# Optimization experiments

Hardware: AMD Instinct MI355X
Metric: run time of the kernel (lower is better)

Reference implementation:

```python
import jax, jax.numpy as jnp
import numpy as np

N = 100000
E = 6400000
IN_CH = 128
HID = 8
HEADS = 2
OUT_CH = 1
NEG_SLOPE = 0.2


def gat_conv(x, src, dst, W, a_src, a_dst, bias, heads, out_ch, concat, n_nodes):
    # x: [N, F_in], W: [F_in, heads*out_ch], a_src/a_dst: [heads, out_ch]
    h = (x @ W).reshape(n_nodes, heads, out_ch)          # [N, H, C]
    alpha_s = jnp.sum(h * a_src[None], axis=-1)          # [N, H]
    alpha_d = jnp.sum(h * a_dst[None], axis=-1)          # [N, H]
    alpha = alpha_s[src] + alpha_d[dst]                  # [E, H]
    alpha = jax.nn.leaky_relu(alpha, NEG_SLOPE)
    # segment softmax over incoming edges of each destination node
    seg_max = jax.ops.segment_max(alpha, dst, num_segments=n_nodes)  # [N, H]
    alpha = jnp.exp(alpha - seg_max[dst])
    denom = jax.ops.segment_sum(alpha, dst, num_segments=n_nodes)    # [N, H]
    alpha = alpha / (denom[dst] + 1e-16)
    msg = h[src] * alpha[..., None]                       # [E, H, C]
    out = jax.ops.segment_sum(msg, dst, num_segments=n_nodes)        # [N, H, C]
    if concat:
        out = out.reshape(n_nodes, heads * out_ch)
    else:
        out = out.mean(axis=1)
    return out + bias


def setup_inputs() -> dict:
    key = jax.random.key(0)
    ks = jax.random.split(key, 12)
    x = jax.random.normal(ks[0], (N, IN_CH), dtype=jnp.float32)
    edge_index = jax.random.randint(ks[1], (2, E), 0, N, dtype=jnp.int64)
    s1 = 1.0 / np.sqrt(IN_CH)
    W1 = jax.random.normal(ks[2], (IN_CH, HEADS * HID), dtype=jnp.float32) * s1
    a_src1 = jax.random.normal(ks[3], (HEADS, HID), dtype=jnp.float32) * (1.0 / np.sqrt(HID))
    a_dst1 = jax.random.normal(ks[4], (HEADS, HID), dtype=jnp.float32) * (1.0 / np.sqrt(HID))
    b1 = jnp.zeros((HEADS * HID,), dtype=jnp.float32)
    s2 = 1.0 / np.sqrt(HEADS * HID)
    W2 = jax.random.normal(ks[5], (HEADS * HID, OUT_CH), dtype=jnp.float32) * s2
    a_src2 = jax.random.normal(ks[6], (1, OUT_CH), dtype=jnp.float32)
    a_dst2 = jax.random.normal(ks[7], (1, OUT_CH), dtype=jnp.float32)
    b2 = jnp.zeros((OUT_CH,), dtype=jnp.float32)
    return {"x": x, "edge_index": edge_index, "W1": W1, "a_src1": a_src1,
            "a_dst1": a_dst1, "b1": b1, "W2": W2, "a_src2": a_src2,
            "a_dst2": a_dst2, "b2": b2}


def reference(x, edge_index, W1, a_src1, a_dst1, b1, W2, a_src2, a_dst2, b2):
    # add self-loops (PyG GATConv default)
    loops = jnp.arange(N, dtype=edge_index.dtype)
    src = jnp.concatenate([edge_index[0], loops])
    dst = jnp.concatenate([edge_index[1], loops])
    h = gat_conv(x, src, dst, W1, a_src1, a_dst1, b1, HEADS, HID, True, N)
    h = jax.nn.relu(h)
    out = gat_conv(h, src, dst, W2, a_src2, a_dst2, b2, 1, OUT_CH, False, N)
    return out
```

## Files before the change

### kernel.cpp

```cpp
#include <hip/hip_runtime.h>
#include <hip/hip_fp16.h>
#include <cstdint>
#include <cstddef>

#define N_NODES 100000
#define E_EDGES 6400000
#define E_TOT   (E_EDGES + N_NODES)
#define IN_CH   128
#define NHID    16
#define RECB    64
#define BSHIFT  8
#define BSZ     256
#define NBUCK   391
#define CHUNK   6144
#define BCAP    24
#define NCHUNK  ((E_TOT + CHUNK - 1) / CHUNK)
#define LCAP    18176

__global__ void k_detect(const int* __restrict__ edge, int* __restrict__ flag) {
    if (blockIdx.x == 0 && threadIdx.x == 0) {
        int odd_or = 0;
        for (int i = 0; i < 64; i++) odd_or |= edge[2 * i + 1];
        flag[0] = (odd_or == 0) ? 1 : 0;
    }
}

__global__ __launch_bounds__(256) void k_gemm1(
        const float* __restrict__ x, const float* __restrict__ W1,
        const float* __restrict__ a_src1, const float* __restrict__ a_dst1,
        char* __restrict__ rec, float* __restrict__ adst) {
    __shared__ __align__(16) float sW[IN_CH * NHID];
    __shared__ __align__(16) float sx[16][132];
    __shared__ float sh[16][17];
    int t = threadIdx.x;
    int r = t >> 4, c = t & 15;
    int row = blockIdx.x * 16 + r;

    const float4* W4 = (const float4*)W1;
    ((float4*)sW)[t] = W4[t];
    ((float4*)sW)[t + 256] = W4[t + 256];

    if (row < N_NODES) {
        const float4* xr = (const float4*)(x + (size_t)row * IN_CH);
        float4 v0 = xr[c];
        float4 v1 = xr[c + 16];
        *(float4*)&sx[r][4 * c] = v0;
        *(float4*)&sx[r][64 + 4 * c] = v1;
    }
    __syncthreads();

    float acc = 0.f;
    if (row < N_NODES) {
        #pragma unroll 16
        for (int k = 0; k < IN_CH; k++) acc = fmaf(sx[r][k], sW[k * NHID + c], acc);
        ((__half*)(rec + (size_t)row * RECB))[c] = __float2half(acc);
    }
    sh[r][c] = acc;
    __syncthreads();

    if (row < N_NODES && c < 4) {
        int h = c & 1;
        const float* av = (c >= 2) ? a_dst1 : a_src1;
        float s = 0.f;
        #pragma unroll
        for (int q = 0; q < 8; q++) s = fmaf(sh[r][h * 8 + q], av[h * 8 + q], s);
        if (c < 2) ((float*)(rec + (size_t)row * RECB + 32))[c] = s;
        else       adst[2 * (size_t)row + (c - 2)] = s;
    }
}

__global__ __launch_bounds__(256) void k_ccount(const int* __restrict__ edge,
                                                const int* __restrict__ flag,
                                                int* __restrict__ ccnt) {
    __shared__ int sc[NBUCK];
    int m64 = flag[0];
    int t = threadIdx.x;
    for (int i = t; i < NBUCK; i += 256) sc[i] = 0;
    __syncthreads();
    size_t c0 = (size_t)blockIdx.x * CHUNK;
    size_t cend = c0 + CHUNK; if (cend > E_TOT) cend = E_TOT;
    size_t ee = (cend < (size_t)E_EDGES) ? cend : (size_t)E_EDGES;

    if (m64) {
        const int4* dp = (const int4*)(edge + 2 * (size_t)E_EDGES);
        for (size_t i = c0 + 2 * t; i < ee; i += 512) {
            int4 v = dp[i >> 1];
            atomicAdd(&sc[v.x >> BSHIFT], 1);
            if (i + 1 < ee) atomicAdd(&sc[v.z >> BSHIFT], 1);
        }
    } else {
        const int4* dp = (const int4*)(edge + (size_t)E_EDGES);
        for (size_t i = c0 + 4 * t; i < ee; i += 1024) {
            int4 v = dp[i >> 2];
            atomicAdd(&sc[v.x >> BSHIFT], 1);
            if (i + 1 < ee) atomicAdd(&sc[v.y >> BSHIFT], 1);
            if (i + 2 < ee) atomicAdd(&sc[v.z >> BSHIFT], 1);
            if (i + 3 < ee) atomicAdd(&sc[v.w >> BSHIFT], 1);
        }
    }
    size_t sl0 = (c0 > (size_t)E_EDGES) ? c0 : (size_t)E_EDGES;
    for (size_t i = sl0 + t; i < cend; i += 256) {
        int d = (int)(i - E_EDGES);
        atomicAdd(&sc[d >> BSHIFT], 1);
    }
    __syncthreads();
    for (int i = t; i < NBUCK; i += 256)
        ccnt[(size_t)blockIdx.x * NBUCK + i] = sc[i];
}

__global__ __launch_bounds__(256) void k_cscan(int* __restrict__ ccnt,
                                               int* __restrict__ bcnt) {
    __shared__ int sd[256];
    __shared__ int carry;
    int b = blockIdx.x, t = threadIdx.x;
    if (t == 0) carry = 0;
    __syncthreads();
    for (int base = 0; base < NCHUNK; base += 256) {
        int c = base + t;
        int v = (c < NCHUNK) ? ccnt[(size_t)c * NBUCK + b] : 0;
        sd[t] = v;
        __syncthreads();
        for (int ofs = 1; ofs < 256; ofs <<= 1) {
            int a = sd[t];
            int bb = (t >= ofs) ? sd[t - ofs] : 0;
            __syncthreads();
            sd[t] = a + bb;
            __syncthreads();
        }
        if (c < NCHUNK) ccnt[(size_t)c * NBUCK + b] = sd[t] - v + carry;
        __syncthreads();
        if (t == 255) carry += sd[255];
        __syncthreads();
    }
    if (t == 0) bcnt[b] = carry;
}

__global__ __launch_bounds__(512) void k_bscan(const int* __restrict__ bcnt,
                                               int* __restrict__ bbase) {
    __shared__ int sd[512];
    int t = threadIdx.x;
    int v = (t < NBUCK) ? bcnt[t] : 0;
    sd[t] = v;
    __syncthreads();
    for (int ofs = 1; ofs < 512; ofs <<= 1) {
        int a = sd[t];
        int b = (t >= ofs) ? sd[t - ofs] : 0;
        __syncthreads();
        sd[t] = a + b;
        __syncthreads();
    }
    if (t < NBUCK) bbase[t] = sd[t] - v;
    if (t == NBUCK) bbase[NBUCK] = sd[NBUCK - 1];
}

__global__ __launch_bounds__(256) void k_bin(const int* __restrict__ edge,
                                             const int* __restrict__ flag,
                                             const int* __restrict__ ccnt,
                                             const int* __restrict__ bbase,
                                             unsigned* __restrict__ staged) {
    __shared__ unsigned lbin[NBUCK][BCAP];
    __shared__ int lcnt[NBUCK];
    __shared__ int lbase[NBUCK];
    int m64 = flag[0];
    int t = threadIdx.x;
    int g = t >> 4, lane = t & 15;

    size_t c0 = (size_t)blockIdx.x * CHUNK;
    if (c0 >= E_TOT) return;
    size_t cend = c0 + CHUNK; if (cend > E_TOT) cend = E_TOT;
    size_t ee = (cend < (size_t)E_EDGES) ? cend : (size_t)E_EDGES;

    for (int i = t; i < NBUCK; i += 256) {
        lcnt[i] = 0;
        lbase[i] = bbase[i] + ccnt[(size_t)blockIdx.x * NBUCK + i];
    }
    __syncthreads();

    auto put = [&](int s, int d) {
        int b = d >> BSHIFT;
        unsigned v = (unsigned)s | ((unsigned)(d & (BSZ - 1)) << 17);
        int idx = atomicAdd(&lcnt[b], 1);
        if (idx < BCAP) lbin[b][idx] = v;
        else            staged[lbase[b] + idx] = v;
    };

    if (m64) {
        const int4* sp = (const int4*)edge;
        const int4* dp = (const int4*)(edge + 2 * (size_t)E_EDGES);
        for (size_t i = c0 + 2 * t; i < ee; i += 512) {
            int4 sv = sp[i >> 1];
            int4 dv = dp[i >> 1];
            put(sv.x, dv.x);
            if (i + 1 < ee) put(sv.z, dv.z);
        }
    } else {
        const int4* sp = (const int4*)edge;
        const int4* dp = (const int4*)(edge + (size_t)E_EDGES);
        for (size_t i = c0 + 4 * t; i < ee; i += 1024) {
            int4 sv = sp[i >> 2];
            int4 dv = dp[i >> 2];
            put(sv.x, dv.x);
            if (i + 1 < ee) put(sv.y, dv.y);
            if (i + 2 < ee) put(sv.z, dv.z);
            if (i + 3 < ee) put(sv.w, dv.w);
        }
    }
    size_t sl0 = (c0 > (size_t)E_EDGES) ? c0 : (size_t)E_EDGES;
    for (size_t i = sl0 + t; i < cend; i += 256) {
        int d = (int)(i - E_EDGES);
        put(d, d);
    }
    __syncthreads();
    for (int b = g; b < NBUCK; b += 16) {
        int n = min(lcnt[b], BCAP);
        if (!n) continue;
        int pos = lbase[b];
        for (int i = lane; i < n; i += 16) staged[pos + i] = lbin[b][i];
    }
}

__global__ __launch_bounds__(512) void k_fused1(
        const unsigned* __restrict__ staged, const int* __restrict__ bbase,
        const char* __restrict__ rec, const float* __restrict__ adst,
        const float* __restrict__ b1, const float* __restrict__ W2,
        int* __restrict__ csr, int* __restrict__ offs,
        float* __restrict__ h2out) {
    __shared__ int lcsr[LCAP];
    __shared__ int hist[BSZ];
    __shared__ int segbeg[BSZ];
    __shared__ int cur[BSZ];
    __shared__ float2 sadp[BSZ];
    int bkt = blockIdx.x;
    int t = threadIdx.x;
    int dbase = bkt << BSHIFT;
    int beg = bbase[bkt], end = bbase[bkt + 1];

    if (t < BSZ) {
        hist[t] = 0;
        int d = dbase + t;
        sadp[t] = (d < N_NODES) ? ((const float2*)adst)[d] : make_float2(0.f, 0.f);
    }
    __syncthreads();
    for (int e = beg + t; e < end; e += 512)
        atomicAdd(&hist[staged[e] >> 17], 1);
    __syncthreads();

    int myv = (t < BSZ) ? hist[t] : 0;
    __syncthreads();
    for (int ofs = 1; ofs < BSZ; ofs <<= 1) {
        int a = 0, b = 0;
        if (t < BSZ) { a = hist[t]; b = (t >= ofs) ? hist[t - ofs] : 0; }
        __syncthreads();
        if (t < BSZ) hist[t] = a + b;
        __syncthreads();
    }
    if (t < BSZ) {
        int excl = hist[t] - myv;
        segbeg[t] = excl;
        cur[t] = excl;
        int d = dbase + t;
        if (d < N_NODES) offs[d] = beg + excl;
    }
    if (bkt == NBUCK - 1 && t == 0) offs[N_NODES] = E_TOT;
    __syncthreads();

    for (int e = beg + t; e < end; e += 512) {
        unsigned v = staged[e];
        int pos = atomicAdd(&cur[v >> 17], 1);
        lcsr[pos] = (int)(v & 0x1FFFFu);
    }
    __syncthreads();

    int n = end - beg;
    for (int i = t; i < n; i += 512) csr[beg + i] = lcsr[i];

    int p = t >> 1, sub = t & 1;
    int sb = segbeg[p], se = cur[p];
    float adpv = sub ? sadp[p].y : sadp[p].x;

    float acc[8];
    #pragma unroll
    for (int c = 0; c < 8; c++) acc[c] = 0.f;
    float den = 0.f;

    auto loadslot = [&](int i, float& aspv, float4& hv) {
        if (i < se) {
            int s = lcsr[i];
            const char* rp = rec + (size_t)s * RECB;
            hv = *(const float4*)(rp + sub * 16);
            aspv = *(const float*)(rp + 32 + 4 * sub);
        }
    };
    auto consume = [&](float aspv, const float4& hv) {
        float a = aspv + adpv; a = (a > 0.f) ? a : 0.2f * a;
        float pw = __expf(a);
        den += pw;
        const __half2* hh = (const __half2*)&hv;
        #pragma unroll
        for (int q = 0; q < 4; q++) {
            float2 f = __half22float2(hh[q]);
            acc[2 * q]     = fmaf(pw, f.x, acc[2 * q]);
            acc[2 * q + 1] = fmaf(pw, f.y, acc[2 * q + 1]);
        }
    };

    float aA = 0.f, aB = 0.f, aC = 0.f, aD = 0.f;
    float4 z4 = make_float4(0.f, 0.f, 0.f, 0.f);
    float4 hA = z4, hB = z4, hC = z4, hD = z4;

    int i = sb;
    loadslot(i,     aA, hA);
    loadslot(i + 1, aB, hB);
    loadslot(i + 2, aC, hC);
    loadslot(i + 3, aD, hD);
    while (true) {
        if (i >= se) break;
        consume(aA, hA); loadslot(i + 4, aA, hA); i++;
        if (i >= se) break;
        consume(aB, hB); loadslot(i + 4, aB, hB); i++;
        if (i >= se) break;
        consume(aC, hC); loadslot(i + 4, aC, hC); i++;
        if (i >= se) break;
        consume(aD, hD); loadslot(i + 4, aD, hD); i++;
    }

    float inv = 1.f / (den + 1e-16f);
    float v = 0.f;
    #pragma unroll
    for (int ch = 0; ch < 8; ch++) {
        float o = acc[ch] * inv + b1[8 * sub + ch];
        o = (o > 0.f) ? o : 0.f;
        v = fmaf(o, W2[8 * sub + ch], v);
    }
    v += __shfl_xor(v, 1, 64);
    if (sub == 0) {
        int d = dbase + p;
        if (d < N_NODES) h2out[d] = v;
    }
}

__global__ __launch_bounds__(256) void k_edge2(
        const int* __restrict__ offs, const int* __restrict__ csr,
        const float* __restrict__ h2,
        const float* __restrict__ a_src2, const float* __restrict__ a_dst2,
        const float* __restrict__ b2, float* __restrict__ out) {
    int t = threadIdx.x;
    int g = t >> 4, lane = t & 15;
    int d = blockIdx.x * 16 + g;
    if (d >= N_NODES) return;

    float as2 = a_src2[0], ad2 = a_dst2[0];
    float adv = h2[d] * ad2;
    int beg = offs[d], end = offs[d + 1];

    float den = 0.f, acc = 0.f;
    auto ls = [&](int ee, float& hs) { if (ee < end) hs = h2[csr[ee]]; };
    auto cs = [&](float hs) {
        float a = fmaf(hs, as2, adv);
        a = (a > 0.f) ? a : 0.2f * a;
        float p = __expf(a);
        den += p;
        acc = fmaf(p, hs, acc);
    };
    float hA = 0.f, hB = 0.f, hC = 0.f, hD = 0.f, hE = 0.f, hF = 0.f;
    int e = beg + lane;
    ls(e, hA); ls(e + 16, hB); ls(e + 32, hC);
    ls(e + 48, hD); ls(e + 64, hE); ls(e + 80, hF);
    while (true) {
        if (e >= end) break;
        cs(hA); ls(e + 96, hA); e += 16;
        if (e >= end) break;
        cs(hB); ls(e + 96, hB); e += 16;
        if (e >= end) break;
        cs(hC); ls(e + 96, hC); e += 16;
        if (e >= end) break;
        cs(hD); ls(e + 96, hD); e += 16;
        if (e >= end) break;
        cs(hE); ls(e + 96, hE); e += 16;
        if (e >= end) break;
        cs(hF); ls(e + 96, hF); e += 16;
    }
    #pragma unroll
    for (int m = 1; m < 16; m <<= 1) {
        den += __shfl_xor(den, m, 64);
        acc += __shfl_xor(acc, m, 64);
    }
    if (lane == 0) out[d] = acc / (den + 1e-16f) + b2[0];
}

extern "C" void kernel_launch(void* const* d_in, const int* in_sizes, int n_in,
                              void* d_out, int out_size, void* d_ws, size_t ws_size,
                              hipStream_t stream) {
    const float* x      = (const float*)d_in[0];
    const int*   edge   = (const int*)  d_in[1];
    const float* W1     = (const float*)d_in[2];
    const float* a_src1 = (const float*)d_in[3];
    const float* a_dst1 = (const float*)d_in[4];
    const float* b1     = (const float*)d_in[5];
    const float* W2     = (const float*)d_in[6];
    const float* a_src2 = (const float*)d_in[7];
    const float* a_dst2 = (const float*)d_in[8];
    const float* b2     = (const float*)d_in[9];

    constexpr size_t A = 256;
    auto al = [](size_t b) { return (b + A - 1) / A * A; };
    char* ws = (char*)d_ws;
    size_t off = 0;
    int*      flag   = (int*)(ws + off);      off += al(256);
    int*      ccnt   = (int*)(ws + off);      off += al((size_t)NCHUNK * NBUCK * 4);
    int*      bcnt   = (int*)(ws + off);      off += al(NBUCK * 4);
    int*      bbase  = (int*)(ws + off);      off += al((NBUCK + 1) * 4);
    unsigned* staged = (unsigned*)(ws + off); off += al((size_t)E_TOT * 4);
    int*      csr    = (int*)(ws + off);      off += al((size_t)E_TOT * 4);
    int*      offs   = (int*)(ws + off);      off += al((size_t)(N_NODES + 1) * 4);
    char*     rec    = (char*)(ws + off);     off += al((size_t)N_NODES * RECB);
    float*    adst   = (float*)(ws + off);    off += al((size_t)N_NODES * 2 * 4);
    float*    h2     = (float*)(ws + off);    off += al((size_t)N_NODES * 4);
    (void)ws_size; (void)in_sizes; (void)n_in; (void)out_size;

    k_detect<<<1, 64, 0, stream>>>(edge, flag);
    k_gemm1 <<<(N_NODES + 15) / 16, 256, 0, stream>>>(x, W1, a_src1, a_dst1, rec, adst);
    k_ccount<<<NCHUNK, 256, 0, stream>>>(edge, flag, ccnt);
    k_cscan <<<NBUCK, 256, 0, stream>>>(ccnt, bcnt);
    k_bscan <<<1, 512, 0, stream>>>(bcnt, bbase);
    k_bin   <<<NCHUNK, 256, 0, stream>>>(edge, flag, ccnt, bbase, staged);
    k_fused1<<<NBUCK, 512, 0, stream>>>(staged, bbase, rec, adst, b1, W2, csr, offs, h2);
    k_edge2 <<<(N_NODES + 15) / 16, 256, 0, stream>>>(offs, csr, h2, a_src2, a_dst2, b2,
                                                      (float*)d_out);
}
```

Baseline: 201.8 us.

## Split node records into compact arrays and use smaller buckets with four lanes per node

Replaces the 64-byte padded per-node record with a dense 32-byte fp16 feature array plus a separate float2 source-score array, which cuts the bytes touched per gathered edge. Halves the destination bucket size to 128 nodes, giving twice as many blocks in the fused aggregation kernel, and uses four threads per node with four channels each. Chunk, bin capacity and scan sizes are retuned to match, and a second shuffle reduces across the four lanes. Each source gather now takes two separate loads instead of one record load, and the binning kernel keeps more, smaller buckets in shared memory.

After: 222.1 us. 1.1x slower.

```diff
diff --git a/kernel.cpp b/kernel.cpp
--- a/kernel.cpp
+++ b/kernel.cpp
@@ -8,14 +8,13 @@
 #define E_TOT   (E_EDGES + N_NODES)
 #define IN_CH   128
 #define NHID    16
-#define RECB    64
-#define BSHIFT  8
-#define BSZ     256
-#define NBUCK   391
-#define CHUNK   6144
-#define BCAP    24
+#define BSHIFT  7
+#define BSZ     128
+#define NBUCK   782
+#define CHUNK   4096
+#define BCAP    12
 #define NCHUNK  ((E_TOT + CHUNK - 1) / CHUNK)
-#define LCAP    18176
+#define LCAP    9280
 
 __global__ void k_detect(const int* __restrict__ edge, int* __restrict__ flag) {
     if (blockIdx.x == 0 && threadIdx.x == 0) {
@@ -28,7 +27,8 @@
 __global__ __launch_bounds__(256) void k_gemm1(
         const float* __restrict__ x, const float* __restrict__ W1,
         const float* __restrict__ a_src1, const float* __restrict__ a_dst1,
-        char* __restrict__ rec, float* __restrict__ adst) {
+        __half* __restrict__ h16, float* __restrict__ asrc,
+        float* __restrict__ adst) {
     __shared__ __align__(16) float sW[IN_CH * NHID];
     __shared__ __align__(16) float sx[16][132];
     __shared__ float sh[16][17];
@@ -53,7 +53,7 @@
     if (row < N_NODES) {
         #pragma unroll 16
         for (int k = 0; k < IN_CH; k++) acc = fmaf(sx[r][k], sW[k * NHID + c], acc);
-        ((__half*)(rec + (size_t)row * RECB))[c] = __float2half(acc);
+        h16[(size_t)row * NHID + c] = __float2half(acc);
     }
     sh[r][c] = acc;
     __syncthreads();
@@ -64,7 +64,7 @@
         float s = 0.f;
         #pragma unroll
         for (int q = 0; q < 8; q++) s = fmaf(sh[r][h * 8 + q], av[h * 8 + q], s);
-        if (c < 2) ((float*)(rec + (size_t)row * RECB + 32))[c] = s;
+        if (c < 2) asrc[2 * (size_t)row + c] = s;
         else       adst[2 * (size_t)row + (c - 2)] = s;
     }
 }
@@ -135,14 +135,14 @@
     if (t == 0) bcnt[b] = carry;
 }
 
-__global__ __launch_bounds__(512) void k_bscan(const int* __restrict__ bcnt,
-                                               int* __restrict__ bbase) {
-    __shared__ int sd[512];
+__global__ __launch_bounds__(1024) void k_bscan(const int* __restrict__ bcnt,
+                                                int* __restrict__ bbase) {
+    __shared__ int sd[1024];
     int t = threadIdx.x;
     int v = (t < NBUCK) ? bcnt[t] : 0;
     sd[t] = v;
     __syncthreads();
-    for (int ofs = 1; ofs < 512; ofs <<= 1) {
+    for (int ofs = 1; ofs < 1024; ofs <<= 1) {
         int a = sd[t];
         int b = (t >= ofs) ? sd[t - ofs] : 0;
         __syncthreads();
@@ -221,7 +221,8 @@
 
 __global__ __launch_bounds__(512) void k_fused1(
         const unsigned* __restrict__ staged, const int* __restrict__ bbase,
-        const char* __restrict__ rec, const float* __restrict__ adst,
+        const __half* __restrict__ h16, const float* __restrict__ asrc,
+        const float* __restrict__ adst,
         const float* __restrict__ b1, const float* __restrict__ W2,
         int* __restrict__ csr, int* __restrict__ offs,
         float* __restrict__ h2out) {
@@ -274,39 +275,40 @@
     int n = end - beg;
     for (int i = t; i < n; i += 512) csr[beg + i] = lcsr[i];
 
-    int p = t >> 1, sub = t & 1;
+    int p = t >> 2, q = t & 3;
+    int head = q >> 1;
     int sb = segbeg[p], se = cur[p];
-    float adpv = sub ? sadp[p].y : sadp[p].x;
-
-    float acc[8];
+    float adpv = head ? sadp[p].y : sadp[p].x;
+
+    float acc[4];
     #pragma unroll
-    for (int c = 0; c < 8; c++) acc[c] = 0.f;
+    for (int c = 0; c < 4; c++) acc[c] = 0.f;
     float den = 0.f;
 
-    auto loadslot = [&](int i, float& aspv, float4& hv) {
+    auto loadslot = [&](int i, float& aspv, float2& hv) {
         if (i < se) {
             int s = lcsr[i];
-            const char* rp = rec + (size_t)s * RECB;
-            hv = *(const float4*)(rp + sub * 16);
-            aspv = *(const float*)(rp + 32 + 4 * sub);
+            float2 asp = ((const float2*)asrc)[s];
+            aspv = head ? asp.y : asp.x;
+            hv = *(const float2*)(h16 + (size_t)s * NHID + q * 4);
         }
     };
-    auto consume = [&](float aspv, const float4& hv) {
+    auto consume = [&](float aspv, const float2& hv) {
         float a = aspv + adpv; a = (a > 0.f) ? a : 0.2f * a;
         float pw = __expf(a);
         den += pw;
         const __half2* hh = (const __half2*)&hv;
-        #pragma unroll
-        for (int q = 0; q < 4; q++) {
-            float2 f = __half22float2(hh[q]);
-            acc[2 * q]     = fmaf(pw, f.x, acc[2 * q]);
-            acc[2 * q + 1] = fmaf(pw, f.y, acc[2 * q + 1]);
-        }
+        float2 f0 = __half22float2(hh[0]);
+        float2 f1 = __half22float2(hh[1]);
+        acc[0] = fmaf(pw, f0.x, acc[0]);
+        acc[1] = fmaf(pw, f0.y, acc[1]);
+        acc[2] = fmaf(pw, f1.x, acc[2]);
+        acc[3] = fmaf(pw, f1.y, acc[3]);
     };
 
     float aA = 0.f, aB = 0.f, aC = 0.f, aD = 0.f;
-    float4 z4 = make_float4(0.f, 0.f, 0.f, 0.f);
-    float4 hA = z4, hB = z4, hC = z4, hD = z4;
+    float2 z2 = make_float2(0.f, 0.f);
+    float2 hA = z2, hB = z2, hC = z2, hD = z2;
 
     int i = sb;
     loadslot(i,     aA, hA);
@@ -327,13 +329,14 @@
     float inv = 1.f / (den + 1e-16f);
     float v = 0.f;
     #pragma unroll
-    for (int ch = 0; ch < 8; ch++) {
-        float o = acc[ch] * inv + b1[8 * sub + ch];
+    for (int c = 0; c < 4; c++) {
+        float o = acc[c] * inv + b1[4 * q + c];
         o = (o > 0.f) ? o : 0.f;
-        v = fmaf(o, W2[8 * sub + ch], v);
+        v = fmaf(o, W2[4 * q + c], v);
     }
     v += __shfl_xor(v, 1, 64);
-    if (sub == 0) {
+    v += __shfl_xor(v, 2, 64);
+    if (q == 0) {
         int d = dbase + p;
         if (d < N_NODES) h2out[d] = v;
     }
@@ -413,18 +416,19 @@
     unsigned* staged = (unsigned*)(ws + off); off += al((size_t)E_TOT * 4);
     int*      csr    = (int*)(ws + off);      off += al((size_t)E_TOT * 4);
     int*      offs   = (int*)(ws + off);      off += al((size_t)(N_NODES + 1) * 4);
-    char*     rec    = (char*)(ws + off);     off += al((size_t)N_NODES * RECB);
+    __half*   h16    = (__half*)(ws + off);   off += al((size_t)N_NODES * NHID * 2);
+    float*    asrc   = (float*)(ws + off);    off += al((size_t)N_NODES * 2 * 4);
     float*    adst   = (float*)(ws + off);    off += al((size_t)N_NODES * 2 * 4);
     float*    h2     = (float*)(ws + off);    off += al((size_t)N_NODES * 4);
     (void)ws_size; (void)in_sizes; (void)n_in; (void)out_size;
 
     k_detect<<<1, 64, 0, stream>>>(edge, flag);
-    k_gemm1 <<<(N_NODES + 15) / 16, 256, 0, stream>>>(x, W1, a_src1, a_dst1, rec, adst);
+    k_gemm1 <<<(N_NODES + 15) / 16, 256, 0, stream>>>(x, W1, a_src1, a_dst1, h16, asrc, adst);
     k_ccount<<<NCHUNK, 256, 0, stream>>>(edge, flag, ccnt);
     k_cscan <<<NBUCK, 256, 0, stream>>>(ccnt, bcnt);
-    k_bscan <<<1, 512, 0, stream>>>(bcnt, bbase);
+    k_bscan <<<1, 1024, 0, stream>>>(bcnt, bbase);
     k_bin   <<<NCHUNK, 256, 0, stream>>>(edge, flag, ccnt, bbase, staged);
-    k_fused1<<<NBUCK, 512, 0, stream>>>(staged, bbase, rec, adst, b1, W2, csr, offs, h2);
+    k_fused1<<<NBUCK, 512, 0, stream>>>(staged, bbase, h16, asrc, adst, b1, W2, csr, offs, h2);
     k_edge2 <<<(N_NODES + 15) / 16, 256, 0, stream>>>(offs, csr, h2, a_src2, a_dst2, b2,
                                                       (float*)d_out);
 }
```
